# Kernel optimization log

Hardware: AMD Instinct MI355X
Metric: run time of the kernel (lower is better)

## Reference

```python
import jax, jax.numpy as jnp
import numpy as np

K = 3  # n_components (hardcoded in original fit())
NORM = float(np.sqrt((2.0 * np.pi) ** 3))


def _prob(X, mean, dev):
    # X: [N,H,W,3], mean: [K,H,W,3], dev: [K,H,W] -> prob [N,K,H,W]
    d2 = jnp.sum(jnp.square(X[:, None] - mean[None]), axis=-1)  # [N,K,H,W]
    return jnp.exp(-d2 / (2.0 * jnp.square(dev)[None])) / (NORM * dev[None])


def _fit(frames, n_iter):
    N, H, W, _ = frames.shape
    # init: mean[k] = (k+1)/4, deviation = 1, weight = 1/K (as in original)
    mean = jnp.stack([jnp.full((H, W, 3), (k + 1) / 4.0, jnp.float32) for k in range(K)])
    dev = jnp.ones((K, H, W), jnp.float32)
    weight = jnp.full((K, H, W), 1.0 / K, jnp.float32)

    def step(carry, _):
        weight, mean, dev = carry
        P = _prob(frames, mean, dev)                      # [N,K,H,W]
        R = weight[None] * P
        R = R / jnp.sum(R, axis=1, keepdims=True)         # responsibilities
        Rs = jnp.sum(R, axis=0)                           # [K,H,W]
        w = Rs / N
        m = jnp.einsum('nkhw,nhwc->khwc', R, frames) / Rs[..., None]
        d = jnp.sum(R * jnp.sum(jnp.square(frames[:, None] - m[None]), axis=-1), axis=0) / Rs
        return (w, m, d), None

    (weight, mean, dev), _ = jax.lax.scan(step, (weight, mean, dev), None, length=n_iter)
    ratio = weight / dev
    fg = ratio <= jnp.min(ratio, axis=0)                  # [K,H,W] bool
    return weight, mean, dev, fg


def _process(frame, mean, dev, fg):
    # frame: [H,W,3]
    dist = jnp.sqrt(jnp.sum(jnp.square(frame[None] - mean), axis=-1))  # [K,H,W]
    index = jnp.argmin(dist, axis=0)                                   # [H,W]
    min_dist = jnp.min(dist, axis=0)                                   # [H,W]
    dev_c = jnp.take_along_axis(dev, index[None], axis=0)[0]
    mask1 = min_dist < dev_c * 2.5
    mask2 = jnp.take_along_axis(fg, index[None], axis=0)[0]
    _ = jnp.logical_and(mask1, mask2)  # computed but unused in original return
    # channel 0: original return (mask2 * 255); channel 1: min_dist (differentiable core)
    return jnp.stack([mask2.astype(jnp.float32) * 255.0, min_dist], axis=0)


def setup_inputs() -> dict:
    key = jax.random.key(0)
    k1, k2 = jax.random.split(key)
    frames = jax.random.uniform(k1, (8, 480, 640, 3), dtype=jnp.float32)
    frame = jax.random.uniform(k2, (480, 640, 3), dtype=jnp.float32)
    return {"frames": frames, "frame": frame, "n_iter": 5}


def reference(frames, frame, n_iter):
    weight, mean, dev, fg = _fit(frames, n_iter)
    return _process(frame, mean, dev, fg)
```

## Files before the change

### kernel.cpp

```cpp
#include <hip/hip_runtime.h>
#include <math.h>

#define KC 3
#define NF 8
#define HH 480
#define WW 640
#define HWPIX (HH * WW)

__device__ __forceinline__ float frcp(float x) { return __builtin_amdgcn_rcpf(x); }
__device__ __forceinline__ float fexp2(float x) { return __builtin_amdgcn_exp2f(x); }

__global__ __launch_bounds__(64) void gmm_fit_process_kernel(
    const float* __restrict__ frames,
    const float* __restrict__ frame,
    const int* __restrict__ n_iter_p,
    float* __restrict__ out)
{
    const int p = blockIdx.x * blockDim.x + threadIdx.x;
    if (p >= HWPIX) return;
    const int n_iter = *n_iter_p;

    float X[NF][3];
    float X2[NF];
#pragma unroll
    for (int n = 0; n < NF; ++n) {
        const float* src = frames + (size_t)n * (HWPIX * 3) + (size_t)p * 3;
        X[n][0] = src[0];
        X[n][1] = src[1];
        X[n][2] = src[2];
        X2[n] = X[n][0] * X[n][0] + X[n][1] * X[n][1] + X[n][2] * X[n][2];
    }

    float mean[KC][3], dev[KC], weight[KC];
#pragma unroll
    for (int k = 0; k < KC; ++k) {
        const float m0 = (float)(k + 1) / 4.0f;
        mean[k][0] = m0; mean[k][1] = m0; mean[k][2] = m0;
        dev[k] = 1.0f;
        weight[k] = 1.0f / 3.0f;
    }

    const float INV_NORM = 0.06349363593424097f;
    const float L2E = 1.4426950408889634f;
    const float DEV_FLOOR = 1e-12f;
    const float S_FLOOR = 1e-20f;

    for (int it = 0; it < n_iter; ++it) {
        float A[KC], B[KC], C[KC], c[KC];
#pragma unroll
        for (int k = 0; k < KC; ++k) {
            const float dsafe = fmaxf(dev[k], DEV_FLOOR);
            const float invd = frcp(dsafe);
            const float a2 = -0.5f * L2E * invd * invd;
            const float m2 = mean[k][0] * mean[k][0] + mean[k][1] * mean[k][1]
                           + mean[k][2] * mean[k][2];
            A[k] = a2;
            B[k] = a2 * m2;
            C[k] = -2.0f * a2;
            c[k] = weight[k] * INV_NORM * invd;
        }

        float rs[KC], mx[KC], my[KC], mz[KC], acc2[KC];
#pragma unroll
        for (int k = 0; k < KC; ++k) { rs[k] = mx[k] = my[k] = mz[k] = acc2[k] = 0.0f; }

#pragma unroll
        for (int n = 0; n < NF; ++n) {
            float r[KC], s = 0.0f;
#pragma unroll
            for (int k = 0; k < KC; ++k) {
                const float t = mean[k][0] * X[n][0]
                              + mean[k][1] * X[n][1]
                              + mean[k][2] * X[n][2];
                float e = A[k] * X2[n] + B[k];
                e = C[k] * t + e;
                r[k] = c[k] * fexp2(e);
                s += r[k];
            }
            const float sinv = (s > S_FLOOR) ? frcp(s) : 0.0f;
#pragma unroll
            for (int k = 0; k < KC; ++k) {
                const float rk = r[k] * sinv;
                rs[k] += rk;
                mx[k] += rk * X[n][0];
                my[k] += rk * X[n][1];
                mz[k] += rk * X[n][2];
                acc2[k] += rk * X2[n];
            }
        }

#pragma unroll
        for (int k = 0; k < KC; ++k) {
            if (rs[k] > S_FLOOR) {
                const float invrs = frcp(rs[k]);
                const float m0 = mx[k] * invrs, m1 = my[k] * invrs, m2c = mz[k] * invrs;
                const float mm2 = m0 * m0 + m1 * m1 + m2c * m2c;
                weight[k] = rs[k] * (1.0f / (float)NF);
                mean[k][0] = m0; mean[k][1] = m1; mean[k][2] = m2c;
                dev[k] = acc2[k] * invrs - mm2;
            } else {
                weight[k] = 0.0f;
            }
        }
    }

    float ratio[KC];
    float rmin = 3.402823466e+38f;
#pragma unroll
    for (int k = 0; k < KC; ++k) {
        ratio[k] = weight[k] * frcp(fmaxf(dev[k], DEV_FLOOR));
        rmin = fminf(rmin, ratio[k]);
    }

    const float fx = frame[(size_t)p * 3 + 0];
    const float fy = frame[(size_t)p * 3 + 1];
    const float fz = frame[(size_t)p * 3 + 2];

    float mind = 3.402823466e+38f;
    int index = 0;
#pragma unroll
    for (int k = 0; k < KC; ++k) {
        const float dx = fx - mean[k][0];
        const float dy = fy - mean[k][1];
        const float dz = fz - mean[k][2];
        const float dist = __builtin_amdgcn_sqrtf(dx * dx + dy * dy + dz * dz);
        if (dist < mind) {
            mind = dist;
            index = k;
        }
    }

    float mask = (ratio[index] <= rmin) ? 255.0f : 0.0f;
    if (!isfinite(mind)) mind = 0.0f;

    out[p] = mask;
    out[HWPIX + p] = mind;
}

extern "C" void kernel_launch(void* const* d_in, const int* in_sizes, int n_in,
                              void* d_out, int out_size, void* d_ws, size_t ws_size,
                              hipStream_t stream) {
    const float* frames = (const float*)d_in[0];
    const float* frame  = (const float*)d_in[1];
    const int*   n_iter = (const int*)d_in[2];
    float* out = (float*)d_out;

    const int threads = 64;
    const int blocks = (HWPIX + threads - 1) / threads;
    gmm_fit_process_kernel<<<blocks, threads, 0, stream>>>(frames, frame, n_iter, out);
}
```

Baseline: 29.73 us.

## Process two pixels per thread using packed float2 vector arithmetic

Each thread now handles a pair of adjacent pixels, holding state in two-wide float vectors so the compiler can emit packed FP32 instructions (v_pk_fma/v_pk_mul) for the EM inner loop. Loads become six contiguous floats per frame, and the two outputs are written as 64-bit vector stores. The launch uses half as many threads, which raises register pressure and lowers the number of waves in flight. The transcendental ops (exp2, rcp, sqrt) stay scalar per lane.

```diff
diff --git a/kernel.cpp b/kernel.cpp
--- a/kernel.cpp
+++ b/kernel.cpp
@@ -6,9 +6,17 @@
 #define HH 480
 #define WW 640
 #define HWPIX (HH * WW)
+#define NPAIR (HWPIX / 2)
+
+typedef float v2f __attribute__((ext_vector_type(2)));
 
 __device__ __forceinline__ float frcp(float x) { return __builtin_amdgcn_rcpf(x); }
 __device__ __forceinline__ float fexp2(float x) { return __builtin_amdgcn_exp2f(x); }
+__device__ __forceinline__ v2f rcp2(v2f x) { return (v2f){frcp(x.x), frcp(x.y)}; }
+__device__ __forceinline__ v2f exp2v(v2f x) { return (v2f){fexp2(x.x), fexp2(x.y)}; }
+__device__ __forceinline__ v2f max2(v2f a, float b) { return (v2f){fmaxf(a.x, b), fmaxf(a.y, b)}; }
+__device__ __forceinline__ v2f min2(v2f a, v2f b) { return (v2f){fminf(a.x, b.x), fminf(a.y, b.y)}; }
+__device__ __forceinline__ v2f v2(float s) { return (v2f){s, s}; }
 
 __global__ __launch_bounds__(64) void gmm_fit_process_kernel(
     const float* __restrict__ frames,
@@ -16,28 +24,30 @@
     const int* __restrict__ n_iter_p,
     float* __restrict__ out)
 {
-    const int p = blockIdx.x * blockDim.x + threadIdx.x;
-    if (p >= HWPIX) return;
+    const int pp = blockIdx.x * blockDim.x + threadIdx.x;
+    if (pp >= NPAIR) return;
     const int n_iter = *n_iter_p;
 
-    float X[NF][3];
-    float X2[NF];
+    v2f X[NF][3];
+    v2f X2[NF];
 #pragma unroll
     for (int n = 0; n < NF; ++n) {
-        const float* src = frames + (size_t)n * (HWPIX * 3) + (size_t)p * 3;
-        X[n][0] = src[0];
-        X[n][1] = src[1];
-        X[n][2] = src[2];
+        const float* src = frames + (size_t)n * (HWPIX * 3) + (size_t)pp * 6;
+        const float a0 = src[0], a1 = src[1], a2 = src[2];
+        const float a3 = src[3], a4 = src[4], a5 = src[5];
+        X[n][0] = (v2f){a0, a3};
+        X[n][1] = (v2f){a1, a4};
+        X[n][2] = (v2f){a2, a5};
         X2[n] = X[n][0] * X[n][0] + X[n][1] * X[n][1] + X[n][2] * X[n][2];
     }
 
-    float mean[KC][3], dev[KC], weight[KC];
+    v2f mean[KC][3], dev[KC], weight[KC];
 #pragma unroll
     for (int k = 0; k < KC; ++k) {
         const float m0 = (float)(k + 1) / 4.0f;
-        mean[k][0] = m0; mean[k][1] = m0; mean[k][2] = m0;
-        dev[k] = 1.0f;
-        weight[k] = 1.0f / 3.0f;
+        mean[k][0] = v2(m0); mean[k][1] = v2(m0); mean[k][2] = v2(m0);
+        dev[k] = v2(1.0f);
+        weight[k] = v2(1.0f / 3.0f);
     }
 
     const float INV_NORM = 0.06349363593424097f;
@@ -46,41 +56,43 @@
     const float S_FLOOR = 1e-20f;
 
     for (int it = 0; it < n_iter; ++it) {
-        float A[KC], B[KC], C[KC], c[KC];
+        v2f A[KC], B[KC], C[KC], c[KC];
 #pragma unroll
         for (int k = 0; k < KC; ++k) {
-            const float dsafe = fmaxf(dev[k], DEV_FLOOR);
-            const float invd = frcp(dsafe);
-            const float a2 = -0.5f * L2E * invd * invd;
-            const float m2 = mean[k][0] * mean[k][0] + mean[k][1] * mean[k][1]
-                           + mean[k][2] * mean[k][2];
-            A[k] = a2;
-            B[k] = a2 * m2;
-            C[k] = -2.0f * a2;
-            c[k] = weight[k] * INV_NORM * invd;
+            const v2f invd = rcp2(max2(dev[k], DEV_FLOOR));
+            const v2f a2v = v2(-0.5f * L2E) * invd * invd;
+            const v2f m2 = mean[k][0] * mean[k][0] + mean[k][1] * mean[k][1]
+                         + mean[k][2] * mean[k][2];
+            A[k] = a2v;
+            B[k] = a2v * m2;
+            C[k] = v2(-2.0f) * a2v;
+            c[k] = weight[k] * v2(INV_NORM) * invd;
         }
 
-        float rs[KC], mx[KC], my[KC], mz[KC], acc2[KC];
+        v2f rs[KC], mx[KC], my[KC], mz[KC], acc2[KC];
 #pragma unroll
-        for (int k = 0; k < KC; ++k) { rs[k] = mx[k] = my[k] = mz[k] = acc2[k] = 0.0f; }
+        for (int k = 0; k < KC; ++k) {
+            rs[k] = v2(0.0f); mx[k] = v2(0.0f); my[k] = v2(0.0f);
+            mz[k] = v2(0.0f); acc2[k] = v2(0.0f);
+        }
 
 #pragma unroll
         for (int n = 0; n < NF; ++n) {
-            float r[KC], s = 0.0f;
+            v2f r[KC], s = v2(0.0f);
 #pragma unroll
             for (int k = 0; k < KC; ++k) {
-                const float t = mean[k][0] * X[n][0]
-                              + mean[k][1] * X[n][1]
-                              + mean[k][2] * X[n][2];
-                float e = A[k] * X2[n] + B[k];
+                const v2f t = mean[k][0] * X[n][0] + mean[k][1] * X[n][1]
+                            + mean[k][2] * X[n][2];
+                v2f e = A[k] * X2[n] + B[k];
                 e = C[k] * t + e;
-                r[k] = c[k] * fexp2(e);
+                r[k] = c[k] * exp2v(e);
                 s += r[k];
             }
-            const float sinv = (s > S_FLOOR) ? frcp(s) : 0.0f;
+            const v2f sinv = (v2f){ (s.x > S_FLOOR) ? frcp(s.x) : 0.0f,
+                                    (s.y > S_FLOOR) ? frcp(s.y) : 0.0f };
 #pragma unroll
             for (int k = 0; k < KC; ++k) {
-                const float rk = r[k] * sinv;
+                const v2f rk = r[k] * sinv;
                 rs[k] += rk;
                 mx[k] += rk * X[n][0];
                 my[k] += rk * X[n][1];
@@ -91,50 +103,64 @@
 
 #pragma unroll
         for (int k = 0; k < KC; ++k) {
-            if (rs[k] > S_FLOOR) {
-                const float invrs = frcp(rs[k]);
-                const float m0 = mx[k] * invrs, m1 = my[k] * invrs, m2c = mz[k] * invrs;
-                const float mm2 = m0 * m0 + m1 * m1 + m2c * m2c;
-                weight[k] = rs[k] * (1.0f / (float)NF);
-                mean[k][0] = m0; mean[k][1] = m1; mean[k][2] = m2c;
-                dev[k] = acc2[k] * invrs - mm2;
-            } else {
-                weight[k] = 0.0f;
-            }
+            const v2f invrs = rcp2(rs[k]);
+            const v2f nm0 = mx[k] * invrs;
+            const v2f nm1 = my[k] * invrs;
+            const v2f nm2 = mz[k] * invrs;
+            const v2f mm2 = nm0 * nm0 + nm1 * nm1 + nm2 * nm2;
+            const v2f ndev = acc2[k] * invrs - mm2;
+            const bool ok0 = rs[k].x > S_FLOOR;
+            const bool ok1 = rs[k].y > S_FLOOR;
+            mean[k][0] = (v2f){ ok0 ? nm0.x : mean[k][0].x, ok1 ? nm0.y : mean[k][0].y };
+            mean[k][1] = (v2f){ ok0 ? nm1.x : mean[k][1].x, ok1 ? nm1.y : mean[k][1].y };
+            mean[k][2] = (v2f){ ok0 ? nm2.x : mean[k][2].x, ok1 ? nm2.y : mean[k][2].y };
+            dev[k]     = (v2f){ ok0 ? ndev.x : dev[k].x,   ok1 ? ndev.y : dev[k].y };
+            weight[k] = rs[k] * v2(0.125f);
         }
     }
 
-    float ratio[KC];
-    float rmin = 3.402823466e+38f;
+    v2f ratio[KC];
+    v2f rmin = v2(3.402823466e+38f);
 #pragma unroll
     for (int k = 0; k < KC; ++k) {
-        ratio[k] = weight[k] * frcp(fmaxf(dev[k], DEV_FLOOR));
-        rmin = fminf(rmin, ratio[k]);
+        ratio[k] = weight[k] * rcp2(max2(dev[k], DEV_FLOOR));
+        rmin = min2(rmin, ratio[k]);
     }
 
-    const float fx = frame[(size_t)p * 3 + 0];
-    const float fy = frame[(size_t)p * 3 + 1];
-    const float fz = frame[(size_t)p * 3 + 2];
+    const float* fsrc = frame + (size_t)pp * 6;
+    const float f0 = fsrc[0], f1 = fsrc[1], f2 = fsrc[2];
+    const float f3 = fsrc[3], f4 = fsrc[4], f5 = fsrc[5];
+    const v2f fx = (v2f){f0, f3}, fy = (v2f){f1, f4}, fz = (v2f){f2, f5};
 
-    float mind = 3.402823466e+38f;
-    int index = 0;
+    v2f dist[KC];
 #pragma unroll
     for (int k = 0; k < KC; ++k) {
-        const float dx = fx - mean[k][0];
-        const float dy = fy - mean[k][1];
-        const float dz = fz - mean[k][2];
-        const float dist = __builtin_amdgcn_sqrtf(dx * dx + dy * dy + dz * dz);
-        if (dist < mind) {
-            mind = dist;
-            index = k;
-        }
+        const v2f dx = fx - mean[k][0];
+        const v2f dy = fy - mean[k][1];
+        const v2f dz = fz - mean[k][2];
+        const v2f d2 = dx * dx + dy * dy + dz * dz;
+        dist[k] = (v2f){ __builtin_amdgcn_sqrtf(d2.x), __builtin_amdgcn_sqrtf(d2.y) };
     }
 
-    float mask = (ratio[index] <= rmin) ? 255.0f : 0.0f;
-    if (!isfinite(mind)) mind = 0.0f;
+    float maskv[2], mindv[2];
+#pragma unroll
+    for (int cmp = 0; cmp < 2; ++cmp) {
+        float mind = 3.402823466e+38f;
+        int index = 0;
+#pragma unroll
+        for (int k = 0; k < KC; ++k) {
+            const float d = (cmp == 0) ? dist[k].x : dist[k].y;
+            if (d < mind) { mind = d; index = k; }
+        }
+        const float rat  = (cmp == 0) ? ((index == 0) ? ratio[0].x : (index == 1) ? ratio[1].x : ratio[2].x)
+                                      : ((index == 0) ? ratio[0].y : (index == 1) ? ratio[1].y : ratio[2].y);
+        const float rmn  = (cmp == 0) ? rmin.x : rmin.y;
+        maskv[cmp] = (rat <= rmn) ? 255.0f : 0.0f;
+        mindv[cmp] = isfinite(mind) ? mind : 0.0f;
+    }
 
-    out[p] = mask;
-    out[HWPIX + p] = mind;
+    *reinterpret_cast<v2f*>(out + (size_t)pp * 2)          = (v2f){maskv[0], maskv[1]};
+    *reinterpret_cast<v2f*>(out + HWPIX + (size_t)pp * 2)  = (v2f){mindv[0], mindv[1]};
 }
 
 extern "C" void kernel_launch(void* const* d_in, const int* in_sizes, int n_in,
@@ -146,6 +172,6 @@
     float* out = (float*)d_out;
 
     const int threads = 64;
-    const int blocks = (HWPIX + threads - 1) / threads;
+    const int blocks = (NPAIR + threads - 1) / threads;
     gmm_fit_process_kernel<<<blocks, threads, 0, stream>>>(frames, frame, n_iter, out);
 }
```

New measurement: 25.17 us. -15.3%, faster.
